# Kernel tuning notes

Measured on AMD Instinct MI355X. Metric: run time of the kernel, lower is better.

Reference implementation:

```python
import jax, jax.numpy as jnp
import numpy as np

N = 8192      # nb_nodes
HID = 128     # hid_dim
OUT = 64      # out_dim
E = 262144    # num edges (avg degree 32)
BN_EPS = 1e-5


def setup_inputs() -> dict:
    key = jax.random.key(0)
    ks = jax.random.split(key, 10)
    x = jax.random.normal(ks[0], (N, HID), dtype=jnp.float32)
    adj = jnp.zeros((N, N), dtype=jnp.float32)  # unused by the module's forward
    src = jax.random.randint(ks[1], (E,), 0, N)
    dst = jax.random.randint(ks[2], (E,), 0, N)
    s = 0.05
    fc_w = jax.random.normal(ks[3], (HID, OUT), dtype=jnp.float32) * s
    fc_b = jnp.zeros((OUT,), dtype=jnp.float32)
    w1 = jax.random.normal(ks[4], (HID, HID), dtype=jnp.float32) * s
    w1_b = jnp.zeros((HID,), dtype=jnp.float32)
    w2 = jax.random.normal(ks[5], (HID, OUT), dtype=jnp.float32) * s
    w2_b = jnp.zeros((OUT,), dtype=jnp.float32)
    epsilon = jnp.full((N,), 0.5, dtype=jnp.float32)  # init.constant_(0.5)
    gamma = jnp.ones((OUT,), dtype=jnp.float32)
    beta = jnp.zeros((OUT,), dtype=jnp.float32)
    return {"x": x, "adj": adj, "src": src, "dst": dst,
            "fc_w": fc_w, "fc_b": fc_b, "w1": w1, "w1_b": w1_b,
            "w2": w2, "w2_b": w2_b, "epsilon": epsilon,
            "gamma": gamma, "beta": beta}


def _neighbor_sum(feat, src, dst):
    # DGL copy_src + sum: each dst node sums features of its src neighbors.
    return jax.ops.segment_sum(feat[src], dst, num_segments=N)


def reference(x, adj, src, dst, fc_w, fc_b, w1, w1_b, w2, w2_b, epsilon, gamma, beta):
    # h1 = fc(x)
    h1 = x @ fc_w + fc_b                                  # [N, OUT]
    # layer1: neighbor-sum then linear, ReLU
    h2 = jax.nn.relu(_neighbor_sum(x, src, dst) @ w1 + w1_b)   # [N, HID]
    # layer2: neighbor-sum then linear
    h2 = _neighbor_sum(h2, src, dst) @ w2 + w2_b          # [N, OUT]
    eps = epsilon[:, None]
    h = (1.0 - eps) * h1 + eps * h2                       # [N, OUT]
    ret = (h @ h.T + x @ x.T) * 0.5                       # [N, N]
    # BatchNorm1d (training mode: batch stats, biased variance)
    mean = jnp.mean(h, axis=0)
    var = jnp.var(h, axis=0)
    h_bn = (h - mean) * jax.lax.rsqrt(var + BN_EPS) * gamma + beta
    return ret, h_bn
```

## Files before the change

kernel.cpp:

```cpp
#include <hip/hip_runtime.h>
#include <hip/hip_bf16.h>

#define N_NODES 8192
#define HID 128
#define OUT_F 64
#define E_EDGES 262144
#define KTOT 192
#define LDK 104

typedef __bf16 bf16x8 __attribute__((ext_vector_type(8)));
typedef float  f32x4  __attribute__((ext_vector_type(4)));

__device__ __forceinline__ unsigned short f2bf(float f) {
    unsigned int u = __float_as_uint(f);
    u += 0x7fffu + ((u >> 16) & 1u);
    return (unsigned short)(u >> 16);
}

__global__ void count_k(const int* __restrict__ dst, int* __restrict__ cnt) {
    int e = blockIdx.x * 256 + threadIdx.x;
    if (e < E_EDGES) atomicAdd(&cnt[dst[e]], 1);
}

__global__ void scan_k(const int* __restrict__ cnt, int* __restrict__ off,
                       int* __restrict__ cursor) {
    __shared__ int part[256];
    int tid = threadIdx.x;
    int base = tid * 32;
    int local[32];
    int s = 0;
    #pragma unroll
    for (int j = 0; j < 32; ++j) { local[j] = s; s += cnt[base + j]; }
    part[tid] = s;
    __syncthreads();
    if (tid == 0) {
        int acc = 0;
        for (int i = 0; i < 256; ++i) { int t = part[i]; part[i] = acc; acc += t; }
    }
    __syncthreads();
    int p = part[tid];
    #pragma unroll
    for (int j = 0; j < 32; ++j) {
        int v = p + local[j];
        off[base + j] = v;
        cursor[base + j] = v;
    }
    if (tid == 255) off[N_NODES] = p + s;
}

__global__ void fill_k(const int* __restrict__ src, const int* __restrict__ dst,
                       int* __restrict__ cursor, int* __restrict__ eidx) {
    int e = blockIdx.x * 256 + threadIdx.x;
    if (e >= E_EDGES) return;
    int pos = atomicAdd(&cursor[dst[e]], 1);
    eidx[pos] = src[e];
}

__global__ void gather_sum_k(const float* __restrict__ feat,
                             const int* __restrict__ eidx,
                             const int* __restrict__ off,
                             float* __restrict__ out) {
    int node = blockIdx.x * 4 + (threadIdx.x >> 6);
    int lane = threadIdx.x & 63;
    int beg = off[node], end = off[node + 1];
    float2 a0 = {0.f, 0.f}, a1 = {0.f, 0.f}, a2 = {0.f, 0.f}, a3 = {0.f, 0.f};
    int j = beg;
    for (; j + 4 <= end; j += 4) {
        int s0 = eidx[j], s1 = eidx[j + 1], s2 = eidx[j + 2], s3 = eidx[j + 3];
        float2 v0 = *((const float2*)(feat + (size_t)s0 * HID) + lane);
        float2 v1 = *((const float2*)(feat + (size_t)s1 * HID) + lane);
        float2 v2 = *((const float2*)(feat + (size_t)s2 * HID) + lane);
        float2 v3 = *((const float2*)(feat + (size_t)s3 * HID) + lane);
        a0.x += v0.x; a0.y += v0.y;
        a1.x += v1.x; a1.y += v1.y;
        a2.x += v2.x; a2.y += v2.y;
        a3.x += v3.x; a3.y += v3.y;
    }
    for (; j < end; ++j) {
        int s0 = eidx[j];
        float2 v0 = *((const float2*)(feat + (size_t)s0 * HID) + lane);
        a0.x += v0.x; a0.y += v0.y;
    }
    float2 r;
    r.x = (a0.x + a1.x) + (a2.x + a3.x);
    r.y = (a0.y + a1.y) + (a2.y + a3.y);
    *((float2*)(out + (size_t)node * HID) + lane) = r;
}

__global__ __launch_bounds__(256)
void mlp1_k(const float* __restrict__ ns1,
            const float* __restrict__ w1,
            const float* __restrict__ w1b,
            float* __restrict__ h2) {
    __shared__ float w[64 * HID];
    __shared__ float xs[32 * HID];
    int tid = threadIdx.x;
    int rowbase = blockIdx.x * 32;

    for (int i = tid; i < 1024; i += 256)
        *(float4*)&xs[i * 4] = *(const float4*)&ns1[(size_t)rowbase * HID + i * 4];

    int c = tid & 127, r0 = tid >> 7;
    float acc[16];
    #pragma unroll
    for (int g = 0; g < 16; ++g) acc[g] = 0.0f;

    for (int kh = 0; kh < 2; ++kh) {
        __syncthreads();
        for (int i = tid; i < 2048; i += 256)
            *(float4*)&w[i * 4] = *(const float4*)&w1[(size_t)kh * 8192 + i * 4];
        __syncthreads();
        #pragma unroll
        for (int g = 0; g < 16; ++g) {
            int rr = r0 + g * 2;
            const float* xr = &xs[rr * HID + kh * 64];
            float a = acc[g];
            #pragma unroll 8
            for (int k = 0; k < 64; ++k)
                a += xr[k] * w[k * HID + c];
            acc[g] = a;
        }
    }
    float b = w1b[c];
    #pragma unroll
    for (int g = 0; g < 16; ++g) {
        int rr = r0 + g * 2;
        h2[(size_t)(rowbase + rr) * HID + c] = fmaxf(acc[g] + b, 0.0f);
    }
}

__global__ __launch_bounds__(256)
void fuse_h_k(const float* __restrict__ x,
              const float* __restrict__ ns2,
              const float* __restrict__ fcw,
              const float* __restrict__ fcb,
              const float* __restrict__ w2,
              const float* __restrict__ w2b,
              const float* __restrict__ eps,
              float* __restrict__ h,
              unsigned short* __restrict__ G) {
    __shared__ float wA[64 * OUT_F];
    __shared__ float wB[64 * OUT_F];
    __shared__ float xs[32 * HID];
    __shared__ float nss[32 * HID];
    int tid = threadIdx.x;
    int rowbase = blockIdx.x * 32;

    for (int i = tid; i < 1024; i += 256) {
        *(float4*)&xs[i * 4]  = *(const float4*)&x[(size_t)rowbase * HID + i * 4];
        *(float4*)&nss[i * 4] = *(const float4*)&ns2[(size_t)rowbase * HID + i * 4];
    }

    int c = tid & 63, r0 = tid >> 6;
    float a1[8], a2[8];
    #pragma unroll
    for (int g = 0; g < 8; ++g) { a1[g] = 0.0f; a2[g] = 0.0f; }

    for (int kh = 0; kh < 2; ++kh) {
        __syncthreads();
        for (int i = tid; i < 1024; i += 256) {
            *(float4*)&wA[i * 4] = *(const float4*)&fcw[(size_t)kh * 4096 + i * 4];
            *(float4*)&wB[i * 4] = *(const float4*)&w2[(size_t)kh * 4096 + i * 4];
        }
        __syncthreads();
        #pragma unroll
        for (int g = 0; g < 8; ++g) {
            int rr = r0 + g * 4;
            const float* xr = &xs[rr * HID + kh * 64];
            const float* nr = &nss[rr * HID + kh * 64];
            float s1 = a1[g], s2 = a2[g];
            #pragma unroll 8
            for (int k = 0; k < 64; ++k) {
                float wa = wA[k * OUT_F + c];
                float wb = wB[k * OUT_F + c];
                s1 += xr[k] * wa;
                s2 += nr[k] * wb;
            }
            a1[g] = s1; a2[g] = s2;
        }
    }

    const float SC = 0.70710678f;
    float b1 = fcb[c], b2 = w2b[c];
    #pragma unroll
    for (int g = 0; g < 8; ++g) {
        int rr = r0 + g * 4;
        int r = rowbase + rr;
        float e = eps[r];
        float hv = (1.0f - e) * (a1[g] + b1) + e * (a2[g] + b2);
        h[(size_t)r * OUT_F + c] = hv;
        unsigned short* Gr = G + (size_t)r * KTOT;
        Gr[c] = f2bf(hv * SC);
        Gr[OUT_F + c]      = f2bf(xs[rr * HID + c] * SC);
        Gr[OUT_F + 64 + c] = f2bf(xs[rr * HID + 64 + c] * SC);
    }
}

__global__ void bn_stats_k(const float* __restrict__ h, float* __restrict__ stats) {
    __shared__ float ls[256], lq[256];
    int tid = threadIdx.x;
    int c = tid & 63, r0 = tid >> 6;
    int rowbase = blockIdx.x * 64;
    float s = 0.0f, q = 0.0f;
    for (int rr = r0; rr < 64; rr += 4) {
        float v = h[(size_t)(rowbase + rr) * OUT_F + c];
        s += v; q += v * v;
    }
    ls[tid] = s; lq[tid] = q;
    __syncthreads();
    if (tid < 64) {
        s = ls[tid] + ls[tid + 64] + ls[tid + 128] + ls[tid + 192];
        q = lq[tid] + lq[tid + 64] + lq[tid + 128] + lq[tid + 192];
        atomicAdd(&stats[tid], s);
        atomicAdd(&stats[64 + tid], q);
    }
}

__global__ void bn_apply_k(const float* __restrict__ h,
                           const float* __restrict__ stats,
                           const float* __restrict__ gamma,
                           const float* __restrict__ beta,
                           float* __restrict__ outBN) {
    int idx = blockIdx.x * 256 + threadIdx.x;
    if (idx >= N_NODES * OUT_F) return;
    int c = idx & 63;
    const float inv_n = 1.0f / 8192.0f;
    float m = stats[c] * inv_n;
    float v = stats[64 + c] * inv_n - m * m;
    outBN[idx] = (h[idx] - m) * rsqrtf(v + 1e-5f) * gamma[c] + beta[c];
}

__global__ __launch_bounds__(256, 2)
void big_gemm_k(const unsigned short* __restrict__ G, float* __restrict__ C) {
    __shared__ unsigned short Ap[128 * LDK];
    __shared__ unsigned short Bp[128 * LDK];
    int tid = threadIdx.x;
    int lane = tid & 63, wid = tid >> 6;
    int wm = wid >> 1, wn = wid & 1;
    int row0 = blockIdx.y * 128, col0 = blockIdx.x * 128;

    f32x4 acc[4][4] = {};

    #pragma unroll
    for (int kh = 0; kh < 2; ++kh) {
        for (int i = tid; i < 128 * 12; i += 256) {
            int r = i / 12, cc = i % 12;
            *(uint4*)(&Ap[r * LDK + cc * 8]) =
                *(const uint4*)(G + (size_t)(row0 + r) * KTOT + kh * 96 + cc * 8);
            *(uint4*)(&Bp[r * LDK + cc * 8]) =
                *(const uint4*)(G + (size_t)(col0 + r) * KTOT + kh * 96 + cc * 8);
        }
        __syncthreads();
        int rA = wm * 64 + (lane & 15);
        int rB = wn * 64 + (lane & 15);
        int klane = (lane >> 4) * 8;
        #pragma unroll
        for (int ks = 0; ks < 3; ++ks) {
            bf16x8 af[4], bfr[4];
            #pragma unroll
            for (int t = 0; t < 4; ++t) {
                af[t]  = *(const bf16x8*)(&Ap[(rA + t * 16) * LDK + ks * 32 + klane]);
                bfr[t] = *(const bf16x8*)(&Bp[(rB + t * 16) * LDK + ks * 32 + klane]);
            }
            #pragma unroll
            for (int tm = 0; tm < 4; ++tm)
                #pragma unroll
                for (int tn = 0; tn < 4; ++tn)
                    acc[tm][tn] = __builtin_amdgcn_mfma_f32_16x16x32_bf16(
                        af[tm], bfr[tn], acc[tm][tn], 0, 0, 0);
        }
        __syncthreads();
    }

    int crow = row0 + wm * 64 + (lane >> 4) * 4;
    int ccol = col0 + wn * 64 + (lane & 15);
    #pragma unroll
    for (int tm = 0; tm < 4; ++tm)
        #pragma unroll
        for (int tn = 0; tn < 4; ++tn)
            #pragma unroll
            for (int r = 0; r < 4; ++r)
                C[(size_t)(crow + tm * 16 + r) * N_NODES + (ccol + tn * 16)] =
                    acc[tm][tn][r];
}

extern "C" void kernel_launch(void* const* d_in, const int* in_sizes, int n_in,
                              void* d_out, int out_size, void* d_ws, size_t ws_size,
                              hipStream_t stream) {
    const float* x    = (const float*)d_in[0];
    const int*   src  = (const int*)d_in[2];
    const int*   dst  = (const int*)d_in[3];
    const float* fcw  = (const float*)d_in[4];
    const float* fcb  = (const float*)d_in[5];
    const float* w1   = (const float*)d_in[6];
    const float* w1b  = (const float*)d_in[7];
    const float* w2   = (const float*)d_in[8];
    const float* w2b  = (const float*)d_in[9];
    const float* eps  = (const float*)d_in[10];
    const float* gamma= (const float*)d_in[11];
    const float* beta = (const float*)d_in[12];

    float* ws = (float*)d_ws;
    float* ns1   = ws;
    float* ns2   = ws + 1048576;
    float* h2    = ws + 2097152;
    float* h     = ws + 3145728;
    unsigned short* G = (unsigned short*)(ws + 3670016);
    float* stats = ws + 3670016 + 786432;
    int*   cnt    = (int*)(ws + 3670016 + 786432 + 128);
    int*   off    = cnt + N_NODES;
    int*   cursor = off + N_NODES + 1;
    int*   eidx   = cursor + N_NODES;

    float* ret   = (float*)d_out;
    float* outBN = (float*)d_out + (size_t)N_NODES * N_NODES;

    hipMemsetAsync(cnt, 0, N_NODES * sizeof(int), stream);
    hipMemsetAsync(stats, 0, 128 * sizeof(float), stream);

    dim3 blk(256);

    count_k<<<E_EDGES / 256, blk, 0, stream>>>(dst, cnt);
    scan_k<<<1, blk, 0, stream>>>(cnt, off, cursor);
    fill_k<<<E_EDGES / 256, blk, 0, stream>>>(src, dst, cursor, eidx);

    gather_sum_k<<<N_NODES / 4, blk, 0, stream>>>(x, eidx, off, ns1);
    mlp1_k<<<N_NODES / 32, blk, 0, stream>>>(ns1, w1, w1b, h2);
    gather_sum_k<<<N_NODES / 4, blk, 0, stream>>>(h2, eidx, off, ns2);
    fuse_h_k<<<N_NODES / 32, blk, 0, stream>>>(x, ns2, fcw, fcb, w2, w2b, eps, h, G);
    bn_stats_k<<<N_NODES / 64, blk, 0, stream>>>(h, stats);
    bn_apply_k<<<(N_NODES * OUT_F) / 256, blk, 0, stream>>>(h, stats, gamma, beta, outBN);
    dim3 grid(64, 64);
    big_gemm_k<<<grid, blk, 0, stream>>>(G, ret);
}
```

Before: 535.8 us.

## Reorder GNN linear/aggregate, fuse BN stats, exploit symmetry in big GEMM

Uses linearity to apply w1 and w2 before neighbor aggregation, so the second gather runs over 64-wide features instead of 128. The fc and w1 projections are fused into one pre-pass kernel. Bias, ReLU, the epsilon blend, BN statistics and the G packing are fused into the gather kernels, and the stats memset moves into scan_k. The big h·hᵀ+x·xᵀ GEMM now computes only lower-triangular tiles and writes each off-diagonal tile twice, once transposed with float4 stores. This roughly halves MFMA work, but the transposed write pattern is less coalesced and half the blocks exit immediately.

```diff
diff --git a/kernel.cpp b/kernel.cpp
--- a/kernel.cpp
+++ b/kernel.cpp
@@ -23,9 +23,10 @@
 }
 
 __global__ void scan_k(const int* __restrict__ cnt, int* __restrict__ off,
-                       int* __restrict__ cursor) {
+                       int* __restrict__ cursor, float* __restrict__ stats) {
     __shared__ int part[256];
     int tid = threadIdx.x;
+    if (tid < 128) stats[tid] = 0.0f;
     int base = tid * 32;
     int local[32];
     int s = 0;
@@ -56,25 +57,90 @@
     eidx[pos] = src[e];
 }
 
-__global__ void gather_sum_k(const float* __restrict__ feat,
-                             const int* __restrict__ eidx,
-                             const int* __restrict__ off,
-                             float* __restrict__ out) {
+__global__ __launch_bounds__(256)
+void pre_k(const float* __restrict__ x,
+           const float* __restrict__ fcw, const float* __restrict__ fcb,
+           const float* __restrict__ w1,
+           float* __restrict__ h1, float* __restrict__ y,
+           unsigned short* __restrict__ G) {
+    __shared__ float wS[64 * 192];
+    __shared__ float xs[16 * HID];
+    int tid = threadIdx.x;
+    int rowbase = blockIdx.x * 16;
+
+    for (int i = tid; i < 512; i += 256)
+        *(float4*)&xs[i * 4] = *(const float4*)&x[(size_t)rowbase * HID + i * 4];
+
+    int c = tid & 63, r0 = tid >> 6;
+    float acc[3][4] = {};
+
+    for (int kh = 0; kh < 2; ++kh) {
+        __syncthreads();
+        for (int i = tid; i < 1024; i += 256) {
+            int k = i >> 4, qd = i & 15;
+            *(float4*)&wS[k * 192 + qd * 4] =
+                *(const float4*)&fcw[(size_t)(kh * 64 + k) * 64 + qd * 4];
+        }
+        for (int i = tid; i < 2048; i += 256) {
+            int k = i >> 5, qd = i & 31;
+            *(float4*)&wS[k * 192 + 64 + qd * 4] =
+                *(const float4*)&w1[(size_t)(kh * 64 + k) * 128 + qd * 4];
+        }
+        __syncthreads();
+        #pragma unroll 4
+        for (int k = 0; k < 64; ++k) {
+            float wa = wS[k * 192 + c];
+            float wb = wS[k * 192 + 64 + c];
+            float wc = wS[k * 192 + 128 + c];
+            #pragma unroll
+            for (int g = 0; g < 4; ++g) {
+                float xv = xs[(r0 + 4 * g) * HID + kh * 64 + k];
+                acc[0][g] += xv * wa;
+                acc[1][g] += xv * wb;
+                acc[2][g] += xv * wc;
+            }
+        }
+    }
+    float b = fcb[c];
+    #pragma unroll
+    for (int g = 0; g < 4; ++g) {
+        int r = rowbase + r0 + 4 * g;
+        h1[(size_t)r * OUT_F + c]    = acc[0][g] + b;
+        y[(size_t)r * HID + c]       = acc[1][g];
+        y[(size_t)r * HID + 64 + c]  = acc[2][g];
+    }
+    const float SC = 0.70710678f;
+    for (int i = tid; i < 2048; i += 256) {
+        int r = i >> 7, cc = i & 127;
+        G[(size_t)(rowbase + r) * KTOT + OUT_F + cc] = f2bf(xs[r * HID + cc] * SC);
+    }
+}
+
+__global__ void gather_relu_k(const float* __restrict__ feat,
+                              const int* __restrict__ eidx,
+                              const int* __restrict__ off,
+                              const float* __restrict__ bias,
+                              float* __restrict__ out) {
     int node = blockIdx.x * 4 + (threadIdx.x >> 6);
     int lane = threadIdx.x & 63;
     int beg = off[node], end = off[node + 1];
-    float2 a0 = {0.f, 0.f}, a1 = {0.f, 0.f}, a2 = {0.f, 0.f}, a3 = {0.f, 0.f};
+    float2 a0{0,0}, a1{0,0}, a2{0,0}, a3{0,0}, a4{0,0}, a5{0,0}, a6{0,0}, a7{0,0};
     int j = beg;
-    for (; j + 4 <= end; j += 4) {
-        int s0 = eidx[j], s1 = eidx[j + 1], s2 = eidx[j + 2], s3 = eidx[j + 3];
+    for (; j + 8 <= end; j += 8) {
+        int s0 = eidx[j],     s1 = eidx[j + 1], s2 = eidx[j + 2], s3 = eidx[j + 3];
+        int s4 = eidx[j + 4], s5 = eidx[j + 5], s6 = eidx[j + 6], s7 = eidx[j + 7];
         float2 v0 = *((const float2*)(feat + (size_t)s0 * HID) + lane);
         float2 v1 = *((const float2*)(feat + (size_t)s1 * HID) + lane);
         float2 v2 = *((const float2*)(feat + (size_t)s2 * HID) + lane);
         float2 v3 = *((const float2*)(feat + (size_t)s3 * HID) + lane);
-        a0.x += v0.x; a0.y += v0.y;
-        a1.x += v1.x; a1.y += v1.y;
-        a2.x += v2.x; a2.y += v2.y;
-        a3.x += v3.x; a3.y += v3.y;
+        float2 v4 = *((const float2*)(feat + (size_t)s4 * HID) + lane);
+        float2 v5 = *((const float2*)(feat + (size_t)s5 * HID) + lane);
+        float2 v6 = *((const float2*)(feat + (size_t)s6 * HID) + lane);
+        float2 v7 = *((const float2*)(feat + (size_t)s7 * HID) + lane);
+        a0.x += v0.x; a0.y += v0.y;  a1.x += v1.x; a1.y += v1.y;
+        a2.x += v2.x; a2.y += v2.y;  a3.x += v3.x; a3.y += v3.y;
+        a4.x += v4.x; a4.y += v4.y;  a5.x += v5.x; a5.y += v5.y;
+        a6.x += v6.x; a6.y += v6.y;  a7.x += v7.x; a7.y += v7.y;
     }
     for (; j < end; ++j) {
         int s0 = eidx[j];
@@ -82,137 +148,92 @@
         a0.x += v0.x; a0.y += v0.y;
     }
     float2 r;
-    r.x = (a0.x + a1.x) + (a2.x + a3.x);
-    r.y = (a0.y + a1.y) + (a2.y + a3.y);
+    r.x = ((a0.x + a1.x) + (a2.x + a3.x)) + ((a4.x + a5.x) + (a6.x + a7.x));
+    r.y = ((a0.y + a1.y) + (a2.y + a3.y)) + ((a4.y + a5.y) + (a6.y + a7.y));
+    float2 bb = *((const float2*)bias + lane);
+    r.x = fmaxf(r.x + bb.x, 0.0f);
+    r.y = fmaxf(r.y + bb.y, 0.0f);
     *((float2*)(out + (size_t)node * HID) + lane) = r;
 }
 
 __global__ __launch_bounds__(256)
-void mlp1_k(const float* __restrict__ ns1,
-            const float* __restrict__ w1,
-            const float* __restrict__ w1b,
-            float* __restrict__ h2) {
-    __shared__ float w[64 * HID];
-    __shared__ float xs[32 * HID];
-    int tid = threadIdx.x;
-    int rowbase = blockIdx.x * 32;
-
-    for (int i = tid; i < 1024; i += 256)
-        *(float4*)&xs[i * 4] = *(const float4*)&ns1[(size_t)rowbase * HID + i * 4];
-
-    int c = tid & 127, r0 = tid >> 7;
-    float acc[16];
-    #pragma unroll
-    for (int g = 0; g < 16; ++g) acc[g] = 0.0f;
-
-    for (int kh = 0; kh < 2; ++kh) {
-        __syncthreads();
-        for (int i = tid; i < 2048; i += 256)
-            *(float4*)&w[i * 4] = *(const float4*)&w1[(size_t)kh * 8192 + i * 4];
-        __syncthreads();
+void mlp2_k(const float* __restrict__ h2, const float* __restrict__ w2,
+            float* __restrict__ z) {
+    __shared__ float wS[HID * 64];
+    __shared__ float xs[16 * HID];
+    int tid = threadIdx.x;
+    int rowbase = blockIdx.x * 16;
+    for (int i = tid; i < 512; i += 256)
+        *(float4*)&xs[i * 4] = *(const float4*)&h2[(size_t)rowbase * HID + i * 4];
+    for (int i = tid; i < 2048; i += 256)
+        *(float4*)&wS[i * 4] = *(const float4*)&w2[i * 4];
+    __syncthreads();
+    int c = tid & 63, r0 = tid >> 6;
+    float acc[4] = {};
+    #pragma unroll 4
+    for (int k = 0; k < HID; ++k) {
+        float wv = wS[k * 64 + c];
         #pragma unroll
-        for (int g = 0; g < 16; ++g) {
-            int rr = r0 + g * 2;
-            const float* xr = &xs[rr * HID + kh * 64];
-            float a = acc[g];
-            #pragma unroll 8
-            for (int k = 0; k < 64; ++k)
-                a += xr[k] * w[k * HID + c];
-            acc[g] = a;
-        }
-    }
-    float b = w1b[c];
-    #pragma unroll
-    for (int g = 0; g < 16; ++g) {
-        int rr = r0 + g * 2;
-        h2[(size_t)(rowbase + rr) * HID + c] = fmaxf(acc[g] + b, 0.0f);
-    }
-}
-
-__global__ __launch_bounds__(256)
-void fuse_h_k(const float* __restrict__ x,
-              const float* __restrict__ ns2,
-              const float* __restrict__ fcw,
-              const float* __restrict__ fcb,
-              const float* __restrict__ w2,
-              const float* __restrict__ w2b,
-              const float* __restrict__ eps,
-              float* __restrict__ h,
-              unsigned short* __restrict__ G) {
-    __shared__ float wA[64 * OUT_F];
-    __shared__ float wB[64 * OUT_F];
-    __shared__ float xs[32 * HID];
-    __shared__ float nss[32 * HID];
-    int tid = threadIdx.x;
-    int rowbase = blockIdx.x * 32;
-
-    for (int i = tid; i < 1024; i += 256) {
-        *(float4*)&xs[i * 4]  = *(const float4*)&x[(size_t)rowbase * HID + i * 4];
-        *(float4*)&nss[i * 4] = *(const float4*)&ns2[(size_t)rowbase * HID + i * 4];
-    }
-
-    int c = tid & 63, r0 = tid >> 6;
-    float a1[8], a2[8];
-    #pragma unroll
-    for (int g = 0; g < 8; ++g) { a1[g] = 0.0f; a2[g] = 0.0f; }
-
-    for (int kh = 0; kh < 2; ++kh) {
-        __syncthreads();
-        for (int i = tid; i < 1024; i += 256) {
-            *(float4*)&wA[i * 4] = *(const float4*)&fcw[(size_t)kh * 4096 + i * 4];
-            *(float4*)&wB[i * 4] = *(const float4*)&w2[(size_t)kh * 4096 + i * 4];
-        }
-        __syncthreads();
-        #pragma unroll
-        for (int g = 0; g < 8; ++g) {
-            int rr = r0 + g * 4;
-            const float* xr = &xs[rr * HID + kh * 64];
-            const float* nr = &nss[rr * HID + kh * 64];
-            float s1 = a1[g], s2 = a2[g];
-            #pragma unroll 8
-            for (int k = 0; k < 64; ++k) {
-                float wa = wA[k * OUT_F + c];
-                float wb = wB[k * OUT_F + c];
-                s1 += xr[k] * wa;
-                s2 += nr[k] * wb;
-            }
-            a1[g] = s1; a2[g] = s2;
-        }
-    }
-
+        for (int g = 0; g < 4; ++g)
+            acc[g] += xs[(r0 + 4 * g) * HID + k] * wv;
+    }
+    #pragma unroll
+    for (int g = 0; g < 4; ++g)
+        z[(size_t)(rowbase + r0 + 4 * g) * OUT_F + c] = acc[g];
+}
+
+__global__ void gather_fuse_k(const float* __restrict__ z,
+                              const int* __restrict__ eidx,
+                              const int* __restrict__ off,
+                              const float* __restrict__ h1,
+                              const float* __restrict__ w2b,
+                              const float* __restrict__ eps,
+                              float* __restrict__ h,
+                              unsigned short* __restrict__ G,
+                              float* __restrict__ stats) {
+    __shared__ float red[8][64];
+    int tid = threadIdx.x;
+    int wid = tid >> 6, lane = tid & 63;
+    float s = 0.0f, q = 0.0f;
+    float b = w2b[lane];
     const float SC = 0.70710678f;
-    float b1 = fcb[c], b2 = w2b[c];
-    #pragma unroll
-    for (int g = 0; g < 8; ++g) {
-        int rr = r0 + g * 4;
-        int r = rowbase + rr;
-        float e = eps[r];
-        float hv = (1.0f - e) * (a1[g] + b1) + e * (a2[g] + b2);
-        h[(size_t)r * OUT_F + c] = hv;
-        unsigned short* Gr = G + (size_t)r * KTOT;
-        Gr[c] = f2bf(hv * SC);
-        Gr[OUT_F + c]      = f2bf(xs[rr * HID + c] * SC);
-        Gr[OUT_F + 64 + c] = f2bf(xs[rr * HID + 64 + c] * SC);
-    }
-}
-
-__global__ void bn_stats_k(const float* __restrict__ h, float* __restrict__ stats) {
-    __shared__ float ls[256], lq[256];
-    int tid = threadIdx.x;
-    int c = tid & 63, r0 = tid >> 6;
-    int rowbase = blockIdx.x * 64;
-    float s = 0.0f, q = 0.0f;
-    for (int rr = r0; rr < 64; rr += 4) {
-        float v = h[(size_t)(rowbase + rr) * OUT_F + c];
-        s += v; q += v * v;
-    }
-    ls[tid] = s; lq[tid] = q;
+    for (int t = 0; t < 4; ++t) {
+        int node = blockIdx.x * 16 + wid * 4 + t;
+        int beg = off[node], end = off[node + 1];
+        float a0 = 0, a1 = 0, a2 = 0, a3 = 0, a4 = 0, a5 = 0, a6 = 0, a7 = 0;
+        int j = beg;
+        for (; j + 8 <= end; j += 8) {
+            int s0 = eidx[j],     s1 = eidx[j + 1], s2 = eidx[j + 2], s3 = eidx[j + 3];
+            int s4 = eidx[j + 4], s5 = eidx[j + 5], s6 = eidx[j + 6], s7 = eidx[j + 7];
+            a0 += z[(size_t)s0 * OUT_F + lane];
+            a1 += z[(size_t)s1 * OUT_F + lane];
+            a2 += z[(size_t)s2 * OUT_F + lane];
+            a3 += z[(size_t)s3 * OUT_F + lane];
+            a4 += z[(size_t)s4 * OUT_F + lane];
+            a5 += z[(size_t)s5 * OUT_F + lane];
+            a6 += z[(size_t)s6 * OUT_F + lane];
+            a7 += z[(size_t)s7 * OUT_F + lane];
+        }
+        for (; j < end; ++j)
+            a0 += z[(size_t)eidx[j] * OUT_F + lane];
+        float gs = ((a0 + a1) + (a2 + a3)) + ((a4 + a5) + (a6 + a7));
+        float e = eps[node];
+        float hv = (1.0f - e) * h1[(size_t)node * OUT_F + lane] + e * (gs + b);
+        h[(size_t)node * OUT_F + lane] = hv;
+        G[(size_t)node * KTOT + lane] = f2bf(hv * SC);
+        s += hv;
+        q += hv * hv;
+    }
+    red[wid][lane] = s;
+    red[4 + wid][lane] = q;
     __syncthreads();
     if (tid < 64) {
-        s = ls[tid] + ls[tid + 64] + ls[tid + 128] + ls[tid + 192];
-        q = lq[tid] + lq[tid + 64] + lq[tid + 128] + lq[tid + 192];
-        atomicAdd(&stats[tid], s);
-        atomicAdd(&stats[64 + tid], q);
+        atomicAdd(&stats[tid],
+                  (red[0][tid] + red[1][tid]) + (red[2][tid] + red[3][tid]));
+    } else if (tid < 128) {
+        int l = tid - 64;
+        atomicAdd(&stats[64 + l],
+                  (red[4][l] + red[5][l]) + (red[6][l] + red[7][l]));
     }
 }
 
@@ -232,12 +253,14 @@
 
 __global__ __launch_bounds__(256, 2)
 void big_gemm_k(const unsigned short* __restrict__ G, float* __restrict__ C) {
+    int bx = blockIdx.x, by = blockIdx.y;
+    if (bx > by) return;
     __shared__ unsigned short Ap[128 * LDK];
     __shared__ unsigned short Bp[128 * LDK];
     int tid = threadIdx.x;
     int lane = tid & 63, wid = tid >> 6;
     int wm = wid >> 1, wn = wid & 1;
-    int row0 = blockIdx.y * 128, col0 = blockIdx.x * 128;
+    int row0 = by * 128, col0 = bx * 128;
 
     f32x4 acc[4][4] = {};
 
@@ -282,6 +305,17 @@
             for (int r = 0; r < 4; ++r)
                 C[(size_t)(crow + tm * 16 + r) * N_NODES + (ccol + tn * 16)] =
                     acc[tm][tn][r];
+
+    if (bx != by) {
+        int trow = col0 + wn * 64 + (lane & 15);
+        int tcol = row0 + wm * 64 + (lane >> 4) * 4;
+        #pragma unroll
+        for (int tm = 0; tm < 4; ++tm)
+            #pragma unroll
+            for (int tn = 0; tn < 4; ++tn)
+                *(float4*)&C[(size_t)(trow + tn * 16) * N_NODES + tcol + tm * 16] =
+                    *(const float4*)&acc[tm][tn];
+    }
 }
 
 extern "C" void kernel_launch(void* const* d_in, const int* in_sizes, int n_in,
@@ -301,9 +335,10 @@
     const float* beta = (const float*)d_in[12];
 
     float* ws = (float*)d_ws;
-    float* ns1   = ws;
-    float* ns2   = ws + 1048576;
-    float* h2    = ws + 2097152;
+    float* y     = ws;
+    float* h2    = ws + 1048576;
+    float* h1    = ws + 2097152;
+    float* z     = ws + 2621440;
     float* h     = ws + 3145728;
     unsigned short* G = (unsigned short*)(ws + 3670016);
     float* stats = ws + 3670016 + 786432;
@@ -316,19 +351,18 @@
     float* outBN = (float*)d_out + (size_t)N_NODES * N_NODES;
 
     hipMemsetAsync(cnt, 0, N_NODES * sizeof(int), stream);
-    hipMemsetAsync(stats, 0, 128 * sizeof(float), stream);
 
     dim3 blk(256);
 
     count_k<<<E_EDGES / 256, blk, 0, stream>>>(dst, cnt);
-    scan_k<<<1, blk, 0, stream>>>(cnt, off, cursor);
+    scan_k<<<1, blk, 0, stream>>>(cnt, off, cursor, stats);
     fill_k<<<E_EDGES / 256, blk, 0, stream>>>(src, dst, cursor, eidx);
 
-    gather_sum_k<<<N_NODES / 4, blk, 0, stream>>>(x, eidx, off, ns1);
-    mlp1_k<<<N_NODES / 32, blk, 0, stream>>>(ns1, w1, w1b, h2);
-    gather_sum_k<<<N_NODES / 4, blk, 0, stream>>>(h2, eidx, off, ns2);
-    fuse_h_k<<<N_NODES / 32, blk, 0, stream>>>(x, ns2, fcw, fcb, w2, w2b, eps, h, G);
-    bn_stats_k<<<N_NODES / 64, blk, 0, stream>>>(h, stats);
+    pre_k<<<N_NODES / 16, blk, 0, stream>>>(x, fcw, fcb, w1, h1, y, G);
+    gather_relu_k<<<N_NODES / 4, blk, 0, stream>>>(y, eidx, off, w1b, h2);
+    mlp2_k<<<N_NODES / 16, blk, 0, stream>>>(h2, w2, z);
+    gather_fuse_k<<<N_NODES / 16, blk, 0, stream>>>(z, eidx, off, h1, w2b, eps,
+                                                    h, G, stats);
     bn_apply_k<<<(N_NODES * OUT_F) / 256, blk, 0, stream>>>(h, stats, gamma, beta, outBN);
     dim3 grid(64, 64);
     big_gemm_k<<<grid, blk, 0, stream>>>(G, ret);
```

Result: no change. 529.2 us (-1.2%).
